# Performance work log

Measured on AMD Instinct MI355X. Metric: run time of the kernel, lower is better.

Reference implementation:

```python
import jax, jax.numpy as jnp
import numpy as np

NEG_INF = -1e30  # stand-in for -inf, avoids NaN under masked rows edge cases


def setup_inputs() -> dict:
    key = jax.random.key(0)
    ks = jax.random.split(key, 6)
    H, N, F_IN, HD, F_OUT = 8, 4096, 512, 64, 512
    X = jax.random.normal(ks[0], (H, N, F_IN), dtype=jnp.float32)
    mask = jax.random.randint(ks[1], (H, N, N), 0, 2, dtype=jnp.int32)
    s = 1.0 / np.sqrt(F_IN)
    W_Q = jax.random.normal(ks[2], (H, HD, F_IN), dtype=jnp.float32) * s
    W_K = jax.random.normal(ks[3], (H, HD, F_IN), dtype=jnp.float32) * s
    W_V = jax.random.normal(ks[4], (H, HD, F_IN), dtype=jnp.float32) * s
    W_O = jax.random.normal(ks[5], (F_OUT, H * HD), dtype=jnp.float32) * (1.0 / np.sqrt(H * HD))
    return {"X": X, "mask": mask, "W_Q": W_Q, "W_K": W_K, "W_V": W_V, "W_O": W_O}


def reference(X, mask, W_Q, W_K, W_V, W_O):
    # X: [H, N, F_in]; W_{Q,K,V}: [H, head_dim, F_in] (torch Linear layout: [out,in])
    Q = jnp.einsum('hnf,hdf->hnd', X, W_Q)
    K = jnp.einsum('hnf,hdf->hnd', X, W_K)
    V = jnp.einsum('hnf,hdf->hnd', X, W_V)
    head_dim = K.shape[-1]
    E = jnp.einsum('hnd,hmd->hnm', Q, K) / jnp.sqrt(jnp.float32(head_dim))  # [H,N,N]
    E = jnp.where(mask == 0, jnp.float32(NEG_INF), E)
    A = jax.nn.softmax(E, axis=-1)
    Hout = jnp.einsum('hnm,hmd->hnd', A, V)  # [H, N, head_dim]
    # concat heads along feature dim -> [N, H*head_dim]
    Hcat = jnp.transpose(Hout, (1, 0, 2)).reshape(Hout.shape[1], -1)
    # dropout is identity in eval mode
    return Hcat @ W_O.T  # [N, fan_out]
```

## Files before the change

kernel.cpp:

```cpp
#include <hip/hip_runtime.h>

typedef __bf16 bf16x8 __attribute__((ext_vector_type(8)));
typedef float f32x4 __attribute__((ext_vector_type(4)));
typedef int i32x4 __attribute__((ext_vector_type(4)));

#define MFMA(a, b, c) __builtin_amdgcn_mfma_f32_16x16x32_bf16((a), (b), (c), 0, 0, 0)
#define GLOAD_LDS(g, l) __builtin_amdgcn_global_load_lds( \
    (const __attribute__((address_space(1))) void*)(g),   \
    (__attribute__((address_space(3))) void*)(l), 16, 0, 0)

constexpr int HEADS = 8, SEQ = 4096, FIN = 512, HD = 64, FOUT = 512;
constexpr float QSCALE = 0.18033688011112042f;

__device__ inline bf16x8 cvt8(const float* __restrict__ p) {
    f32x4 a = *(const f32x4*)p;
    f32x4 b = *(const f32x4*)(p + 4);
    bf16x8 r;
    r[0] = (__bf16)a[0]; r[1] = (__bf16)a[1]; r[2] = (__bf16)a[2]; r[3] = (__bf16)a[3];
    r[4] = (__bf16)b[0]; r[5] = (__bf16)b[1]; r[6] = (__bf16)b[2]; r[7] = (__bf16)b[3];
    return r;
}

__global__ __launch_bounds__(256) void qkv_kernel(
    const float* __restrict__ X, const float* __restrict__ Wq,
    const float* __restrict__ Wk, const float* __restrict__ Wv,
    __bf16* __restrict__ Q, __bf16* __restrict__ K, __bf16* __restrict__ Vt)
{
    const int h = blockIdx.y;
    const int tid = threadIdx.x;
    const int w = tid >> 6, lane = tid & 63;
    const int quad = lane >> 4, l16 = lane & 15;
    const int m = blockIdx.x * 64 + w * 16 + l16;

    const float* xrow = X + ((size_t)h * SEQ + m) * FIN + quad * 8;
    const float* wqh = Wq + (size_t)h * HD * FIN + quad * 8;
    const float* wkh = Wk + (size_t)h * HD * FIN + quad * 8;
    const float* wvh = Wv + (size_t)h * HD * FIN + quad * 8;

    const f32x4 vzero = {0.f, 0.f, 0.f, 0.f};
    f32x4 accQ[4], accK[4], accV[4];
#pragma unroll
    for (int t = 0; t < 4; ++t) { accQ[t] = vzero; accK[t] = vzero; accV[t] = vzero; }

    for (int f0 = 0; f0 < FIN; f0 += 32) {
        bf16x8 a = cvt8(xrow + f0);
#pragma unroll
        for (int t = 0; t < 4; ++t) {
            const int wrow = (t * 16 + l16) * FIN + f0;
            bf16x8 bq = cvt8(wqh + wrow);
            bf16x8 bk = cvt8(wkh + wrow);
            bf16x8 bv = cvt8(wvh + wrow);
            accQ[t] = MFMA(a, bq, accQ[t]);
            accK[t] = MFMA(a, bk, accK[t]);
            accV[t] = MFMA(a, bv, accV[t]);
        }
    }

    const int row0 = blockIdx.x * 64 + w * 16 + quad * 4;
#pragma unroll
    for (int t = 0; t < 4; ++t) {
        const int d = t * 16 + l16;
#pragma unroll
        for (int r = 0; r < 4; ++r) {
            const int n = row0 + r;
            Q[((size_t)h * SEQ + n) * HD + d] = (__bf16)(accQ[t][r] * QSCALE);
            K[((size_t)h * SEQ + n) * HD + d] = (__bf16)accK[t][r];
            Vt[((size_t)h * HD + d) * SEQ + n] = (__bf16)accV[t][r];
        }
    }
}

__global__ __launch_bounds__(256) void attn_kernel(
    const __bf16* __restrict__ Q, const __bf16* __restrict__ K,
    const __bf16* __restrict__ Vt, const int* __restrict__ mask,
    __bf16* __restrict__ Hcat)
{
    __shared__ __align__(16) unsigned char lds[65536 + 4 * 2304];

    const int h = blockIdx.y;
    const int tid = threadIdx.x;
    const int w = tid >> 6, lane = tid & 63;
    const int quad = lane >> 4, l16 = lane & 15;
    const int q0b = blockIdx.x * 64;
    const int q0 = q0b + w * 16;

    __bf16* PT = (__bf16*)(lds + 65536) + w * 1152;

    const __bf16* Qh = Q + (size_t)h * SEQ * HD;
    const __bf16* Kh = K + (size_t)h * SEQ * HD;
    const __bf16* Vh = Vt + (size_t)h * HD * SEQ;
    const int* mh = mask + (size_t)h * SEQ * SEQ;

    const int sKV = w * 64 + lane;
    const int sM  = w * 64 + lane;

    auto stage = [&](int n0, int b) {
        unsigned char* bK = lds + 32768 + b * 8192;
        unsigned char* bV = lds + 49152 + b * 8192;
        unsigned char* bM = lds + b * 16384;
        const __bf16* Kn = Kh + (size_t)n0 * HD;
#pragma unroll
        for (int c = 0; c < 2; ++c) {
            const int s = c * 256 + sKV;
            GLOAD_LDS(Kn + s * 8, bK + s * 16);
            GLOAD_LDS(Vh + (size_t)(s >> 3) * SEQ + n0 + (s & 7) * 8, bV + s * 16);
        }
#pragma unroll
        for (int c = 0; c < 4; ++c) {
            const int s = c * 256 + sM;
            GLOAD_LDS(mh + (size_t)(q0b + (s >> 4)) * SEQ + n0 + (s & 15) * 4, bM + s * 16);
        }
    };

    bf16x8 qa0 = *(const bf16x8*)(Qh + (size_t)(q0 + l16) * HD + quad * 8);
    bf16x8 qa1 = *(const bf16x8*)(Qh + (size_t)(q0 + l16) * HD + 32 + quad * 8);

    const f32x4 vzero = {0.f, 0.f, 0.f, 0.f};
    f32x4 O[4];
    float lsum = 0.f;
#pragma unroll
    for (int t = 0; t < 4; ++t) O[t] = vzero;

    stage(0, 0);
    __syncthreads();

    for (int i = 0; i < SEQ / 64; ++i) {
        const int n0 = i * 64;
        const int cur = i & 1;
        if (i + 1 < SEQ / 64) stage(n0 + 64, cur ^ 1);

        const __bf16* cK = (const __bf16*)(lds + 32768 + cur * 8192);
        const __bf16* cV = (const __bf16*)(lds + 49152 + cur * 8192);
        const unsigned char* cM = lds + cur * 16384;

        f32x4 St[4];
#pragma unroll
        for (int t = 0; t < 4; ++t) {
            const int kr = t * 16 + l16;
            bf16x8 kb0 = *(const bf16x8*)(cK + kr * 64 + quad * 8);
            bf16x8 kb1 = *(const bf16x8*)(cK + kr * 64 + 32 + quad * 8);
            St[t] = MFMA(kb0, qa0, vzero);
            St[t] = MFMA(kb1, qa1, St[t]);
        }

#pragma unroll
        for (int t = 0; t < 4; ++t) {
            i32x4 mv = *(const i32x4*)(cM + ((w * 16 + l16) * 64 + t * 16 + quad * 4) * 4);
            union { unsigned long long u; __bf16 hh[4]; } pk;
#pragma unroll
            for (int r = 0; r < 4; ++r) {
                float p = __builtin_amdgcn_exp2f(St[t][r]);
                p = mv[r] ? p : 0.f;
                lsum += p;
                pk.hh[r] = (__bf16)p;
            }
            *(unsigned long long*)(PT + l16 * 72 + t * 16 + quad * 4) = pk.u;
        }

        bf16x8 pa0 = *(const bf16x8*)(PT + l16 * 72 + quad * 8);
        bf16x8 pa1 = *(const bf16x8*)(PT + l16 * 72 + 32 + quad * 8);
#pragma unroll
        for (int t = 0; t < 4; ++t) {
            const int dr = t * 16 + l16;
            bf16x8 vb0 = *(const bf16x8*)(cV + dr * 64 + quad * 8);
            bf16x8 vb1 = *(const bf16x8*)(cV + dr * 64 + 32 + quad * 8);
            O[t] = MFMA(pa0, vb0, O[t]);
            O[t] = MFMA(pa1, vb1, O[t]);
        }
        __syncthreads();
    }

    lsum += __shfl_xor(lsum, 16, 64);
    lsum += __shfl_xor(lsum, 32, 64);
    float inv[4];
#pragma unroll
    for (int r = 0; r < 4; ++r) {
        float Lr = __shfl(lsum, quad * 4 + r, 64);
        inv[r] = Lr > 0.f ? 1.0f / Lr : 0.f;
    }

#pragma unroll
    for (int r = 0; r < 4; ++r) {
        const int n = q0 + quad * 4 + r;
#pragma unroll
        for (int t = 0; t < 4; ++t)
            Hcat[(size_t)n * FOUT + h * HD + t * 16 + l16] = (__bf16)(O[t][r] * inv[r]);
    }
}

__global__ __launch_bounds__(256) void out_kernel(
    const __bf16* __restrict__ Hcat, const float* __restrict__ Wo,
    float* __restrict__ out)
{
    const int tid = threadIdx.x;
    const int w = tid >> 6, lane = tid & 63;
    const int quad = lane >> 4, l16 = lane & 15;
    const int n0 = blockIdx.x * 64 + w * 16;
    const int o0 = blockIdx.y * 64;

    const f32x4 vzero = {0.f, 0.f, 0.f, 0.f};
    f32x4 acc[4];
#pragma unroll
    for (int t = 0; t < 4; ++t) acc[t] = vzero;

    for (int k0 = 0; k0 < FOUT; k0 += 32) {
        bf16x8 a = *(const bf16x8*)(Hcat + (size_t)(n0 + l16) * FOUT + k0 + quad * 8);
#pragma unroll
        for (int t = 0; t < 4; ++t) {
            bf16x8 b = cvt8(Wo + (size_t)(o0 + t * 16 + l16) * FOUT + k0 + quad * 8);
            acc[t] = MFMA(a, b, acc[t]);
        }
    }
#pragma unroll
    for (int t = 0; t < 4; ++t)
#pragma unroll
        for (int r = 0; r < 4; ++r)
            out[(size_t)(n0 + quad * 4 + r) * FOUT + o0 + t * 16 + l16] = acc[t][r];
}

extern "C" void kernel_launch(void* const* d_in, const int* in_sizes, int n_in,
                              void* d_out, int out_size, void* d_ws, size_t ws_size,
                              hipStream_t stream) {
    const float* X    = (const float*)d_in[0];
    const int*   mask = (const int*)d_in[1];
    const float* Wq   = (const float*)d_in[2];
    const float* Wk   = (const float*)d_in[3];
    const float* Wv   = (const float*)d_in[4];
    const float* Wo   = (const float*)d_in[5];
    float* out = (float*)d_out;

    __bf16* Q    = (__bf16*)d_ws;
    __bf16* K    = Q + (size_t)HEADS * SEQ * HD;
    __bf16* Vt   = K + (size_t)HEADS * SEQ * HD;
    __bf16* Hcat = Vt + (size_t)HEADS * HD * SEQ;

    qkv_kernel<<<dim3(SEQ / 64, HEADS), 256, 0, stream>>>(X, Wq, Wk, Wv, Q, K, Vt);
    attn_kernel<<<dim3(SEQ / 64, HEADS), 256, 0, stream>>>(Q, K, Vt, mask, Hcat);
    out_kernel<<<dim3(SEQ / 64, FOUT / 64), 256, 0, stream>>>(Hcat, Wo, out);
}
```

Measured before the change: 911.8 us.

## Load attention mask directly into registers, shrink LDS, interleave heads across blocks

The mask tile now goes straight from global memory into registers, double-buffered across two unrolled tiles, instead of being staged through LDS with async global-to-LDS copies. This roughly halves LDS use per block and adds a launch bound of 3 blocks per SM to raise occupancy. The grid is flattened so consecutive blocks handle different heads for the same query range. The mask stream is the dominant traffic (512MB of int32), so these changes aim to improve latency hiding and bandwidth; the costs are more register pressure and a less coalesced per-row mask access pattern.

```diff
diff --git a/kernel.cpp b/kernel.cpp
--- a/kernel.cpp
+++ b/kernel.cpp
@@ -70,34 +70,33 @@
     }
 }
 
-__global__ __launch_bounds__(256) void attn_kernel(
+__global__ __launch_bounds__(256, 3) void attn_kernel(
     const __bf16* __restrict__ Q, const __bf16* __restrict__ K,
     const __bf16* __restrict__ Vt, const int* __restrict__ mask,
     __bf16* __restrict__ Hcat)
 {
-    __shared__ __align__(16) unsigned char lds[65536 + 4 * 2304];
-
-    const int h = blockIdx.y;
+    __shared__ __align__(16) unsigned char lds[32768 + 4 * 2304];
+
+    const int bid = blockIdx.x;
+    const int h = bid & 7;
+    const int q0b = (bid >> 3) * 64;
     const int tid = threadIdx.x;
     const int w = tid >> 6, lane = tid & 63;
     const int quad = lane >> 4, l16 = lane & 15;
-    const int q0b = blockIdx.x * 64;
     const int q0 = q0b + w * 16;
 
-    __bf16* PT = (__bf16*)(lds + 65536) + w * 1152;
+    __bf16* PT = (__bf16*)(lds + 32768) + w * 1152;
 
     const __bf16* Qh = Q + (size_t)h * SEQ * HD;
     const __bf16* Kh = K + (size_t)h * SEQ * HD;
     const __bf16* Vh = Vt + (size_t)h * HD * SEQ;
-    const int* mh = mask + (size_t)h * SEQ * SEQ;
+    const int* mrow = mask + ((size_t)h * SEQ + q0 + l16) * SEQ + quad * 4;
 
     const int sKV = w * 64 + lane;
-    const int sM  = w * 64 + lane;
 
     auto stage = [&](int n0, int b) {
-        unsigned char* bK = lds + 32768 + b * 8192;
-        unsigned char* bV = lds + 49152 + b * 8192;
-        unsigned char* bM = lds + b * 16384;
+        unsigned char* bK = lds + b * 8192;
+        unsigned char* bV = lds + 16384 + b * 8192;
         const __bf16* Kn = Kh + (size_t)n0 * HD;
 #pragma unroll
         for (int c = 0; c < 2; ++c) {
@@ -105,11 +104,10 @@
             GLOAD_LDS(Kn + s * 8, bK + s * 16);
             GLOAD_LDS(Vh + (size_t)(s >> 3) * SEQ + n0 + (s & 7) * 8, bV + s * 16);
         }
-#pragma unroll
-        for (int c = 0; c < 4; ++c) {
-            const int s = c * 256 + sM;
-            GLOAD_LDS(mh + (size_t)(q0b + (s >> 4)) * SEQ + n0 + (s & 15) * 4, bM + s * 16);
-        }
+    };
+    auto loadM = [&](int n0, i32x4* mv) {
+#pragma unroll
+        for (int t = 0; t < 4; ++t) mv[t] = *(const i32x4*)(mrow + n0 + t * 16);
     };
 
     bf16x8 qa0 = *(const bf16x8*)(Qh + (size_t)(q0 + l16) * HD + quad * 8);
@@ -121,17 +119,20 @@
 #pragma unroll
     for (int t = 0; t < 4; ++t) O[t] = vzero;
 
+    i32x4 mA[4], mB[4];
     stage(0, 0);
+    loadM(0, mA);
     __syncthreads();
 
-    for (int i = 0; i < SEQ / 64; ++i) {
+    auto tile = [&](int i, const i32x4* mc, i32x4* mn) {
         const int n0 = i * 64;
         const int cur = i & 1;
-        if (i + 1 < SEQ / 64) stage(n0 + 64, cur ^ 1);
-
-        const __bf16* cK = (const __bf16*)(lds + 32768 + cur * 8192);
-        const __bf16* cV = (const __bf16*)(lds + 49152 + cur * 8192);
-        const unsigned char* cM = lds + cur * 16384;
+        if (i + 1 < SEQ / 64) {
+            stage(n0 + 64, cur ^ 1);
+            loadM(n0 + 64, mn);
+        }
+        const __bf16* cK = (const __bf16*)(lds + cur * 8192);
+        const __bf16* cV = (const __bf16*)(lds + 16384 + cur * 8192);
 
         f32x4 St[4];
 #pragma unroll
@@ -145,12 +146,11 @@
 
 #pragma unroll
         for (int t = 0; t < 4; ++t) {
-            i32x4 mv = *(const i32x4*)(cM + ((w * 16 + l16) * 64 + t * 16 + quad * 4) * 4);
             union { unsigned long long u; __bf16 hh[4]; } pk;
 #pragma unroll
             for (int r = 0; r < 4; ++r) {
                 float p = __builtin_amdgcn_exp2f(St[t][r]);
-                p = mv[r] ? p : 0.f;
+                p = mc[t][r] ? p : 0.f;
                 lsum += p;
                 pk.hh[r] = (__bf16)p;
             }
@@ -168,6 +168,11 @@
             O[t] = MFMA(pa1, vb1, O[t]);
         }
         __syncthreads();
+    };
+
+    for (int i = 0; i < SEQ / 64; i += 2) {
+        tile(i, mA, mB);
+        tile(i + 1, mB, mA);
     }
 
     lsum += __shfl_xor(lsum, 16, 64);
@@ -235,6 +240,6 @@
     __bf16* Hcat = Vt + (size_t)HEADS * HD * SEQ;
 
     qkv_kernel<<<dim3(SEQ / 64, HEADS), 256, 0, stream>>>(X, Wq, Wk, Wv, Q, K, Vt);
-    attn_kernel<<<dim3(SEQ / 64, HEADS), 256, 0, stream>>>(Q, K, Vt, mask, Hcat);
+    attn_kernel<<<(SEQ / 64) * HEADS, 256, 0, stream>>>(Q, K, Vt, mask, Hcat);
     out_kernel<<<dim3(SEQ / 64, FOUT / 64), 256, 0, stream>>>(Hcat, Wo, out);
 }
```

New measurement: 895.2 us. Within noise of the previous version (-1.8%).
